# Kernel optimization log

Measured on AMD Instinct MI355X. Metric: run time of the kernel, lower is better.

The kernel has to match this reference:

```python
import jax, jax.numpy as jnp
import numpy as np

# Perfect-forest re-expression of FeatureRNN's recursive tree message passing.
K, B, D = 2048, 4, 5                       # graphs (roots), branching factor, depth
ATOM, BOND, HID, OUT = 125, 12, 125, 40    # module defaults
SIZES = [K * B**d for d in range(D)]       # nodes per level: [2048,8192,32768,131072,524288]
NOFF = [0] + list(np.cumsum(SIZES))        # node offsets per level in flat node_msg
BOFF = [0] + list(np.cumsum(SIZES[1:]))    # edge offsets: bonds stored for levels 1..D-1
N_TOTAL = int(sum(SIZES))                  # 698368
E_TOTAL = N_TOTAL - K                      # 696320


def setup_inputs() -> dict:
    key = jax.random.key(0)
    k0, k1, k2, k3 = jax.random.split(key, 4)
    return {
        "node_msg": jax.random.normal(k0, (N_TOTAL, ATOM), jnp.float32),
        "bonds": jax.random.normal(k1, (E_TOTAL, BOND), jnp.float32),
        "W1": jax.random.normal(k2, (ATOM + BOND + OUT, HID), jnp.float32) * 0.05,
        "b1": jnp.zeros((HID,), jnp.float32),
        "W2": jax.random.normal(k3, (HID, OUT), jnp.float32) * 0.05,
        "b2": jnp.zeros((OUT,), jnp.float32),
    }


def _net(x, W1, b1, W2, b2):
    # nn.Sequential(Linear, LeakyReLU(0.01), Linear, LeakyReLU(0.01))
    h = jax.nn.leaky_relu(x @ W1 + b1, 0.01)
    return jax.nn.leaky_relu(h @ W2 + b2, 0.01)


def reference(node_msg, bonds, W1, b1, W2, b2):
    # Leaves: net(cat[msg, zeros(bond+out)])
    leaf_msg = node_msg[NOFF[D - 1]:NOFF[D]]                       # [n_leaf, ATOM]
    pad = jnp.zeros((SIZES[D - 1], BOND + OUT), node_msg.dtype)
    out = _net(jnp.concatenate([leaf_msg, pad], axis=1), W1, b1, W2, b2)
    # Level-synchronous upward pass (structural loop over D-1 tree levels)
    for d in range(D - 2, -1, -1):
        n_p = SIZES[d]
        msg_p = node_msg[NOFF[d]:NOFF[d + 1]]                      # [n_p, ATOM]
        bond = bonds[BOFF[d]:BOFF[d + 1]]                          # [n_p*B, BOND]
        inp = jnp.concatenate(
            [jnp.repeat(msg_p, B, axis=0), bond, out], axis=1)     # [n_p*B, 177]
        # per-parent sum over contiguous children == cat(...).sum(dim=0)
        out = _net(inp, W1, b1, W2, b2).reshape(n_p, B, OUT).sum(axis=1)
    return out  # [K, OUT]
```

## Files before the change

kernel.cpp:

```cpp
#include <hip/hip_runtime.h>
#include <hip/hip_bf16.h>
#include <cstddef>


typedef __attribute__((ext_vector_type(8))) _Float16 h8;
typedef __attribute__((ext_vector_type(4))) float f32x4;
typedef __attribute__((ext_vector_type(4))) unsigned int v4u;

static constexpr int HID = 125, OUT = 40;

__device__ __forceinline__ unsigned short f2h(float x) {
    _Float16 h = (_Float16)x;
    return __builtin_bit_cast(unsigned short, h);
}
__device__ __forceinline__ unsigned int pkh(float a, float b) {
    return (unsigned int)f2h(a) | ((unsigned int)f2h(b) << 16);
}

__global__ void prep_w(const float* __restrict__ W1, const float* __restrict__ W2,
                       unsigned short* __restrict__ w1g, unsigned int* __restrict__ w2f) {
    if (blockIdx.x < 96) {
        int idx = blockIdx.x * 256 + threadIdx.x;
        int j = idx & 7, ln = (idx >> 3) & 63, mt = (idx >> 9) & 7, kc = idx >> 12;
        int hid = mt * 16 + (ln & 15);
        int kp = kc * 32 + ((ln >> 4) << 3) + j;
        int k = (kp < 125) ? kp
              : (kp >= 128 && kp < 140) ? kp - 3
              : (kp >= 144 && kp < 184) ? kp - 7 : -1;
        float v = (k >= 0 && hid < HID) ? W1[(size_t)k * HID + hid] : 0.f;
        w1g[idx] = f2h(v);
    } else {
        int t = threadIdx.x;
        for (int task = t; task < 12 * 64; task += 256) {
            int ln = task & 63, fr = task >> 6;
            int kt = fr / 3, qt = fr % 3;
            int q = qt * 16 + (ln & 15);
            unsigned int w[4];
#pragma unroll
            for (int jp = 0; jp < 4; jp++) {
                unsigned short e[2];
#pragma unroll
                for (int s = 0; s < 2; s++) {
                    int j = jp * 2 + s;
                    int hid = kt * 32 + ((j >> 2) << 4) + ((ln >> 4) << 2) + (j & 3);
                    float v = (hid < HID && q < OUT) ? W2[(size_t)hid * OUT + q] : 0.f;
                    e[s] = f2h(v);
                }
                w[jp] = (unsigned int)e[0] | ((unsigned int)e[1] << 16);
            }
            v4u val = {w[0], w[1], w[2], w[3]};
            ((v4u*)w2f)[fr * 64 + ln] = val;
        }
    }
}

__global__ void __launch_bounds__(256, 3)
leaf_k(const float* __restrict__ msg, const unsigned short* __restrict__ w1g,
       const unsigned int* __restrict__ w2f,
       const float* __restrict__ b1, const float* __restrict__ b2,
       unsigned short* __restrict__ outp) {
    __shared__ float Xs[4][2][32 * 36];

    const int tid = threadIdx.x;
    const int lane = tid & 63;
    const int wv = tid >> 6;
    const int l15 = tid & 15;
    const int l16 = (tid >> 4) & 3;
    const int sr = lane >> 5;
    const int sc = lane & 31;
    const int row0 = blockIdx.x * 128 + wv * 32;

    float xa[16], xb[16];

    auto issueA = [&](int j) {
        const int col = j * 32 + sc;
        const bool ok = col < 125;
#pragma unroll
        for (int q = 0; q < 16; q++)
            xa[q] = ok ? msg[(size_t)(row0 + 2 * q + sr) * 125 + col] : 0.f;
    };
    auto issueB = [&](int j) {
        const int col = j * 32 + sc;
        const bool ok = col < 125;
#pragma unroll
        for (int q = 0; q < 16; q++)
            xb[q] = ok ? msg[(size_t)(row0 + 2 * q + sr) * 125 + col] : 0.f;
    };
    auto writeA = [&](int b) {
#pragma unroll
        for (int q = 0; q < 16; q++) Xs[wv][b][(2 * q + sr) * 36 + sc] = xa[q];
    };
    auto writeB = [&](int b) {
#pragma unroll
        for (int q = 0; q < 16; q++) Xs[wv][b][(2 * q + sr) * 36 + sc] = xb[q];
    };

    f32x4 acc[8][2];
#pragma unroll
    for (int mt = 0; mt < 8; mt++) {
        f32x4 bi;
#pragma unroll
        for (int r = 0; r < 4; r++) {
            int h_ = mt * 16 + l16 * 4 + r;
            bi[r] = (h_ < HID) ? b1[h_] : 0.f;
        }
        acc[mt][0] = bi;
        acc[mt][1] = bi;
    }

    auto mfma_chunk = [&](int j, int b) {
        h8 xf[2];
#pragma unroll
        for (int nt = 0; nt < 2; ++nt) {
            const float* rp = &Xs[wv][b][(nt * 16 + l15) * 36 + l16 * 8];
            float t[8];
#pragma unroll
            for (int i = 0; i < 8; i++) t[i] = rp[i];
            v4u xv = {pkh(t[0], t[1]), pkh(t[2], t[3]),
                      pkh(t[4], t[5]), pkh(t[6], t[7])};
            xf[nt] = __builtin_bit_cast(h8, xv);
        }
#pragma unroll
        for (int mt = 0; mt < 8; ++mt) {
            h8 wf = *(const h8*)&w1g[(size_t)((j * 8 + mt) * 64 + lane) * 8];
            acc[mt][0] = __builtin_amdgcn_mfma_f32_16x16x32_f16(wf, xf[0], acc[mt][0], 0, 0, 0);
            acc[mt][1] = __builtin_amdgcn_mfma_f32_16x16x32_f16(wf, xf[1], acc[mt][1], 0, 0, 0);
        }
    };

    issueA(0);
    writeA(0);
    issueB(1);
    issueA(2);
    mfma_chunk(0, 0);
    writeB(1);
    issueB(3);
    mfma_chunk(1, 1);
    writeA(0);
    mfma_chunk(2, 0);
    writeB(1);
    mfma_chunk(3, 1);

#pragma unroll
    for (int mt = 0; mt < 8; mt++)
#pragma unroll
        for (int nt = 0; nt < 2; nt++)
#pragma unroll
            for (int r = 0; r < 4; r++)
                acc[mt][nt][r] = fmaxf(acc[mt][nt][r], 0.01f * acc[mt][nt][r]);

    float b2v[3];
#pragma unroll
    for (int qt = 0; qt < 3; qt++) {
        int q = qt * 16 + l15;
        b2v[qt] = (q < OUT) ? b2[q] : 0.f;
    }

    unsigned short* s16 = (unsigned short*)&Xs[wv][0][0];
#pragma unroll
    for (int nt = 0; nt < 2; ++nt) {
        h8 A[4];
#pragma unroll
        for (int kt = 0; kt < 4; kt++) {
            v4u av = {pkh(acc[2 * kt][nt][0], acc[2 * kt][nt][1]),
                      pkh(acc[2 * kt][nt][2], acc[2 * kt][nt][3]),
                      pkh(acc[2 * kt + 1][nt][0], acc[2 * kt + 1][nt][1]),
                      pkh(acc[2 * kt + 1][nt][2], acc[2 * kt + 1][nt][3])};
            A[kt] = __builtin_bit_cast(h8, av);
        }
#pragma unroll
        for (int qt = 0; qt < 3; ++qt) {
            f32x4 o = {0.f, 0.f, 0.f, 0.f};
#pragma unroll
            for (int kt = 0; kt < 4; kt++) {
                v4u wvv = ((const v4u*)w2f)[(kt * 3 + qt) * 64 + lane];
                o = __builtin_amdgcn_mfma_f32_16x16x32_f16(
                    A[kt], __builtin_bit_cast(h8, wvv), o, 0, 0, 0);
            }
            int q = qt * 16 + l15;
            if (q < OUT) {
#pragma unroll
                for (int r = 0; r < 4; r++) {
                    int rl = nt * 16 + l16 * 4 + r;
                    float v = o[r] + b2v[qt];
                    v = fmaxf(v, 0.01f * v);
                    s16[rl * 40 + q] = f2h(v);
                }
            }
        }
    }
    {
        v4u* gdst = (v4u*)(outp + (size_t)row0 * 40);
        const v4u* s4 = (const v4u*)s16;
#pragma unroll
        for (int i = 0; i < 3; i++) {
            int u = lane + i * 64;
            if (i < 2 || u < 160) gdst[u] = s4[u];
        }
    }
}

template <int MODE>
__global__ void __launch_bounds__(256, 4)
mid_k(const float* __restrict__ msg, const float* __restrict__ bonds,
      const unsigned short* __restrict__ child,
      const unsigned short* __restrict__ w1g, const unsigned int* __restrict__ w2f,
      const float* __restrict__ b1, const float* __restrict__ b2,
      void* __restrict__ outp) {
    __shared__ float MS[4][1000];
    __shared__ float BS[4][384];
    __shared__ unsigned short CS[4][1280];

    const int tid = threadIdx.x;
    const int lane = tid & 63;
    const int wv = tid >> 6;
    const int l15 = tid & 15;
    const int l16 = (tid >> 4) & 3;
    const int row0 = blockIdx.x * 128 + wv * 32;
    const int par0 = row0 >> 2;

    {
        const f32x4* sm = (const f32x4*)(msg + (size_t)par0 * 125);
        f32x4* dm = (f32x4*)&MS[wv][0];
#pragma unroll
        for (int i = 0; i < 4; i++) {
            int u = lane + i * 64;
            if (i < 3 || u < 250) dm[u] = sm[u];
        }
        const f32x4* sb = (const f32x4*)(bonds + (size_t)row0 * 12);
        f32x4* db = (f32x4*)&BS[wv][0];
#pragma unroll
        for (int i = 0; i < 2; i++) {
            int u = lane + i * 64;
            if (i < 1 || u < 96) db[u] = sb[u];
        }
        const v4u* sc = (const v4u*)(child + (size_t)row0 * 40);
        v4u* dc = (v4u*)&CS[wv][0];
#pragma unroll
        for (int i = 0; i < 3; i++) {
            int u = lane + i * 64;
            if (i < 2 || u < 160) dc[u] = sc[u];
        }
    }

    f32x4 acc[8][2];
#pragma unroll
    for (int mt = 0; mt < 8; mt++) {
        f32x4 bi;
#pragma unroll
        for (int r = 0; r < 4; r++) {
            int h_ = mt * 16 + l16 * 4 + r;
            bi[r] = (h_ < HID) ? b1[h_] : 0.f;
        }
        acc[mt][0] = bi;
        acc[mt][1] = bi;
    }

#pragma unroll
    for (int j = 0; j < 6; ++j) {
        h8 xf[2];
#pragma unroll
        for (int nt = 0; nt < 2; ++nt) {
            const int rl = nt * 16 + l15;
            if (j < 4) {
                const float* pp = &MS[wv][(rl >> 2) * 125];
                const int k0 = j * 32 + l16 * 8;
                float t[8];
#pragma unroll
                for (int i = 0; i < 8; i++) {
                    int col = k0 + i;
                    int cs = (col < 125) ? col : 0;
                    float v = pp[cs];
                    t[i] = (col < 125) ? v : 0.f;
                }
                v4u xv = {pkh(t[0], t[1]), pkh(t[2], t[3]), pkh(t[4], t[5]), pkh(t[6], t[7])};
                xf[nt] = __builtin_bit_cast(h8, xv);
            } else if (j == 4) {
                if (l16 < 2) {
                    const float* bp = &BS[wv][rl * 12];
                    float t[8];
#pragma unroll
                    for (int i = 0; i < 8; i++) {
                        int c = l16 * 8 + i;
                        int cs = (c < 12) ? c : 0;
                        float v = bp[cs];
                        t[i] = (c < 12) ? v : 0.f;
                    }
                    v4u xv = {pkh(t[0], t[1]), pkh(t[2], t[3]), pkh(t[4], t[5]), pkh(t[6], t[7])};
                    xf[nt] = __builtin_bit_cast(h8, xv);
                } else {
                    xf[nt] = *(const h8*)&CS[wv][rl * 40 + (l16 - 2) * 8];
                }
            } else {
                if (l16 < 3) {
                    xf[nt] = *(const h8*)&CS[wv][rl * 40 + 16 + l16 * 8];
                } else {
                    h8 z = {};
                    xf[nt] = z;
                }
            }
        }
#pragma unroll
        for (int mt = 0; mt < 8; ++mt) {
            h8 wf = *(const h8*)&w1g[(size_t)((j * 8 + mt) * 64 + lane) * 8];
            acc[mt][0] = __builtin_amdgcn_mfma_f32_16x16x32_f16(wf, xf[0], acc[mt][0], 0, 0, 0);
            acc[mt][1] = __builtin_amdgcn_mfma_f32_16x16x32_f16(wf, xf[1], acc[mt][1], 0, 0, 0);
        }
    }

#pragma unroll
    for (int mt = 0; mt < 8; mt++)
#pragma unroll
        for (int nt = 0; nt < 2; nt++)
#pragma unroll
            for (int r = 0; r < 4; r++)
                acc[mt][nt][r] = fmaxf(acc[mt][nt][r], 0.01f * acc[mt][nt][r]);

    float b2v[3];
#pragma unroll
    for (int qt = 0; qt < 3; qt++) {
        int q = qt * 16 + l15;
        b2v[qt] = (q < OUT) ? b2[q] : 0.f;
    }
#pragma unroll
    for (int nt = 0; nt < 2; ++nt) {
        h8 A[4];
#pragma unroll
        for (int kt = 0; kt < 4; kt++) {
            v4u av = {pkh(acc[2 * kt][nt][0], acc[2 * kt][nt][1]),
                      pkh(acc[2 * kt][nt][2], acc[2 * kt][nt][3]),
                      pkh(acc[2 * kt + 1][nt][0], acc[2 * kt + 1][nt][1]),
                      pkh(acc[2 * kt + 1][nt][2], acc[2 * kt + 1][nt][3])};
            A[kt] = __builtin_bit_cast(h8, av);
        }
#pragma unroll
        for (int qt = 0; qt < 3; ++qt) {
            f32x4 o = {0.f, 0.f, 0.f, 0.f};
#pragma unroll
            for (int kt = 0; kt < 4; kt++) {
                v4u wvv = ((const v4u*)w2f)[(kt * 3 + qt) * 64 + lane];
                o = __builtin_amdgcn_mfma_f32_16x16x32_f16(
                    A[kt], __builtin_bit_cast(h8, wvv), o, 0, 0, 0);
            }
            int q = qt * 16 + l15;
            float s = 0.f;
#pragma unroll
            for (int r = 0; r < 4; r++) {
                float v = o[r] + b2v[qt];
                s += fmaxf(v, 0.01f * v);
            }
            if (q < OUT) {
                int p = par0 + nt * 4 + l16;
                if (MODE == 1)
                    ((unsigned short*)outp)[(size_t)p * 40 + q] = f2h(s);
                else
                    ((float*)outp)[(size_t)p * 40 + q] = s;
            }
        }
    }
}

extern "C" void kernel_launch(void* const* d_in, const int* in_sizes, int n_in,
                              void* d_out, int out_size, void* d_ws, size_t ws_size,
                              hipStream_t stream) {
    const float* node_msg = (const float*)d_in[0];
    const float* bonds = (const float*)d_in[1];
    const float* W1 = (const float*)d_in[2];
    const float* b1 = (const float*)d_in[3];
    const float* W2 = (const float*)d_in[4];
    const float* b2 = (const float*)d_in[5];
    float* out = (float*)d_out;

    char* ws = (char*)d_ws;
    unsigned short* bufA = (unsigned short*)ws;
    unsigned short* bufB = (unsigned short*)(ws + 41943040);
    unsigned short* w1g = (unsigned short*)(ws + 52428800);
    unsigned int* w2f = (unsigned int*)(ws + 52428800 + 49152);

    prep_w<<<97, 256, 0, stream>>>(W1, W2, w1g, w2f);

    leaf_k<<<4096, 256, 0, stream>>>(
        node_msg + (size_t)175104 * 125, w1g, w2f, b1, b2, bufA);
    mid_k<1><<<4096, 256, 0, stream>>>(
        node_msg + (size_t)43008 * 125, bonds + (size_t)172032 * 12, bufA,
        w1g, w2f, b1, b2, bufB);
    mid_k<1><<<1024, 256, 0, stream>>>(
        node_msg + (size_t)10240 * 125, bonds + (size_t)40960 * 12, bufB,
        w1g, w2f, b1, b2, bufA);
    mid_k<1><<<256, 256, 0, stream>>>(
        node_msg + (size_t)2048 * 125, bonds + (size_t)8192 * 12, bufA,
        w1g, w2f, b1, b2, bufB);
    mid_k<2><<<64, 256, 0, stream>>>(
        node_msg, bonds, bufB, w1g, w2f, b1, b2, out);
}
```

Before: 194.8 us.

## Stage leaf input as fp16 in LDS and overlap mid-kernel bond/child loads

In the leaf kernel, input rows are converted to fp16 when written to shared memory, so the MFMA fragments are read with a single vector load instead of eight float reads and packs. This halves LDS use, and the occupancy hint is raised from 3 to 4 blocks. In the mid kernel, the global loads for messages, bonds and child outputs are all issued into registers up front. Only the message tile is stored to LDS before the first four MFMA chunks, and the bond/child stores are deferred until after them so that load latency overlaps compute. This costs extra registers that may pressure occupancy, and an unused 'tb' variable is added.

```diff
diff --git a/kernel.cpp b/kernel.cpp
--- a/kernel.cpp
+++ b/kernel.cpp
@@ -54,12 +54,12 @@
     }
 }
 
-__global__ void __launch_bounds__(256, 3)
+__global__ void __launch_bounds__(256, 4)
 leaf_k(const float* __restrict__ msg, const unsigned short* __restrict__ w1g,
        const unsigned int* __restrict__ w2f,
        const float* __restrict__ b1, const float* __restrict__ b2,
        unsigned short* __restrict__ outp) {
-    __shared__ float Xs[4][2][32 * 36];
+    __shared__ unsigned short Xs[4][2][32 * 40];
 
     const int tid = threadIdx.x;
     const int lane = tid & 63;
@@ -88,11 +88,11 @@
     };
     auto writeA = [&](int b) {
 #pragma unroll
-        for (int q = 0; q < 16; q++) Xs[wv][b][(2 * q + sr) * 36 + sc] = xa[q];
+        for (int q = 0; q < 16; q++) Xs[wv][b][(2 * q + sr) * 40 + sc] = f2h(xa[q]);
     };
     auto writeB = [&](int b) {
 #pragma unroll
-        for (int q = 0; q < 16; q++) Xs[wv][b][(2 * q + sr) * 36 + sc] = xb[q];
+        for (int q = 0; q < 16; q++) Xs[wv][b][(2 * q + sr) * 40 + sc] = f2h(xb[q]);
     };
 
     f32x4 acc[8][2];
@@ -111,15 +111,8 @@
     auto mfma_chunk = [&](int j, int b) {
         h8 xf[2];
 #pragma unroll
-        for (int nt = 0; nt < 2; ++nt) {
-            const float* rp = &Xs[wv][b][(nt * 16 + l15) * 36 + l16 * 8];
-            float t[8];
-#pragma unroll
-            for (int i = 0; i < 8; i++) t[i] = rp[i];
-            v4u xv = {pkh(t[0], t[1]), pkh(t[2], t[3]),
-                      pkh(t[4], t[5]), pkh(t[6], t[7])};
-            xf[nt] = __builtin_bit_cast(h8, xv);
-        }
+        for (int nt = 0; nt < 2; ++nt)
+            xf[nt] = *(const h8*)&Xs[wv][b][(nt * 16 + l15) * 40 + l16 * 8];
 #pragma unroll
         for (int mt = 0; mt < 8; ++mt) {
             h8 wf = *(const h8*)&w1g[(size_t)((j * 8 + mt) * 64 + lane) * 8];
@@ -156,7 +149,7 @@
         b2v[qt] = (q < OUT) ? b2[q] : 0.f;
     }
 
-    unsigned short* s16 = (unsigned short*)&Xs[wv][0][0];
+    unsigned short* s16 = &Xs[wv][0][0];
 #pragma unroll
     for (int nt = 0; nt < 2; ++nt) {
         h8 A[4];
@@ -219,27 +212,35 @@
     const int row0 = blockIdx.x * 128 + wv * 32;
     const int par0 = row0 >> 2;
 
+    f32x4 mreg[4];
+    f32x4 breg[2];
+    v4u creg[3];
     {
         const f32x4* sm = (const f32x4*)(msg + (size_t)par0 * 125);
+#pragma unroll
+        for (int i = 0; i < 4; i++) {
+            int u = lane + i * 64;
+            if (i < 3 || u < 250) mreg[i] = sm[u];
+        }
+        const f32x4* sb = (const f32x4*)(bonds + (size_t)row0 * 12);
+#pragma unroll
+        for (int i = 0; i < 2; i++) {
+            int u = lane + i * 64;
+            if (i < 1 || u < 96) breg[i] = sb[u];
+        }
+        const v4u* sc = (const v4u*)(child + (size_t)row0 * 40);
+#pragma unroll
+        for (int i = 0; i < 3; i++) {
+            int u = lane + i * 64;
+            if (i < 2 || u < 160) creg[i] = sc[u];
+        }
+    }
+    {
         f32x4* dm = (f32x4*)&MS[wv][0];
 #pragma unroll
         for (int i = 0; i < 4; i++) {
             int u = lane + i * 64;
-            if (i < 3 || u < 250) dm[u] = sm[u];
-        }
-        const f32x4* sb = (const f32x4*)(bonds + (size_t)row0 * 12);
-        f32x4* db = (f32x4*)&BS[wv][0];
-#pragma unroll
-        for (int i = 0; i < 2; i++) {
-            int u = lane + i * 64;
-            if (i < 1 || u < 96) db[u] = sb[u];
-        }
-        const v4u* sc = (const v4u*)(child + (size_t)row0 * 40);
-        v4u* dc = (v4u*)&CS[wv][0];
-#pragma unroll
-        for (int i = 0; i < 3; i++) {
-            int u = lane + i * 64;
-            if (i < 2 || u < 160) dc[u] = sc[u];
+            if (i < 3 || u < 250) dm[u] = mreg[i];
         }
     }
 
@@ -257,25 +258,54 @@
     }
 
 #pragma unroll
-    for (int j = 0; j < 6; ++j) {
+    for (int j = 0; j < 4; ++j) {
         h8 xf[2];
 #pragma unroll
         for (int nt = 0; nt < 2; ++nt) {
             const int rl = nt * 16 + l15;
-            if (j < 4) {
-                const float* pp = &MS[wv][(rl >> 2) * 125];
-                const int k0 = j * 32 + l16 * 8;
-                float t[8];
-#pragma unroll
-                for (int i = 0; i < 8; i++) {
-                    int col = k0 + i;
-                    int cs = (col < 125) ? col : 0;
-                    float v = pp[cs];
-                    t[i] = (col < 125) ? v : 0.f;
-                }
-                v4u xv = {pkh(t[0], t[1]), pkh(t[2], t[3]), pkh(t[4], t[5]), pkh(t[6], t[7])};
-                xf[nt] = __builtin_bit_cast(h8, xv);
-            } else if (j == 4) {
+            const float* pp = &MS[wv][(rl >> 2) * 125];
+            const int k0 = j * 32 + l16 * 8;
+            float t[8];
+#pragma unroll
+            for (int i = 0; i < 8; i++) {
+                int col = k0 + i;
+                int cs = (col < 125) ? col : 0;
+                float v = pp[cs];
+                t[i] = (col < 125) ? v : 0.f;
+            }
+            v4u xv = {pkh(t[0], t[1]), pkh(t[2], t[3]), pkh(t[4], t[5]), pkh(t[6], t[7])};
+            xf[nt] = __builtin_bit_cast(h8, xv);
+        }
+#pragma unroll
+        for (int mt = 0; mt < 8; ++mt) {
+            h8 wf = *(const h8*)&w1g[(size_t)((j * 8 + mt) * 64 + lane) * 8];
+            acc[mt][0] = __builtin_amdgcn_mfma_f32_16x16x32_f16(wf, xf[0], acc[mt][0], 0, 0, 0);
+            acc[mt][1] = __builtin_amdgcn_mfma_f32_16x16x32_f16(wf, xf[1], acc[mt][1], 0, 0, 0);
+        }
+    }
+
+    {
+        f32x4* db = (f32x4*)&BS[wv][0];
+#pragma unroll
+        for (int i = 0; i < 2; i++) {
+            int u = lane + i * 64;
+            if (i < 1 || u < 96) db[u] = breg[i];
+        }
+        v4u* dc = (v4u*)&CS[wv][0];
+#pragma unroll
+        for (int i = 0; i < 3; i++) {
+            int u = lane + i * 64;
+            if (i < 2 || u < 160) dc[u] = creg[i];
+        }
+    }
+
+#pragma unroll
+    for (int j = 4; j < 6; ++j) {
+        h8 xf[2];
+#pragma unroll
+        for (int nt = 0; nt < 2; ++nt) {
+            const int rl = nt * 16 + l15;
+            if (j == 4) {
                 if (l16 < 2) {
                     const float* bp = &BS[wv][rl * 12];
                     float t[8];
@@ -333,6 +363,7 @@
                       pkh(acc[2 * kt + 1][nt][2], acc[2 * kt + 1][nt][3])};
             A[kt] = __builtin_bit_cast(h8, av);
         }
+        const int tb = wv * 32 + nt * 16;
 #pragma unroll
         for (int qt = 0; qt < 3; ++qt) {
             f32x4 o = {0.f, 0.f, 0.f, 0.f};
```

Result: slower. 246.2 us (+26.4%).
